# Optimization experiments

Hardware: AMD Instinct MI355X
Metric: run time of the kernel (lower is better)

The kernel has to match this reference:

```python
import jax, jax.numpy as jnp
import numpy as np

NV, NSEG, SEGSZ, GRID = 778, 16, 49, 32
SCALE_FACTOR = 0.1


def grid_sample_3d(vol, pts):
    """Trilinear grid_sample, align_corners=True, zeros padding.
    vol: [D,H,W]; pts: [N,3] with (x,y,z) in [-1,1] (x indexes W, z indexes D).
    """
    D, H, W = vol.shape
    fx = (pts[:, 0] + 1.0) * 0.5 * (W - 1)
    fy = (pts[:, 1] + 1.0) * 0.5 * (H - 1)
    fz = (pts[:, 2] + 1.0) * 0.5 * (D - 1)
    x0f, y0f, z0f = jnp.floor(fx), jnp.floor(fy), jnp.floor(fz)
    wx, wy, wz = fx - x0f, fy - y0f, fz - z0f
    x0 = x0f.astype(jnp.int32)
    y0 = y0f.astype(jnp.int32)
    z0 = z0f.astype(jnp.int32)
    out = jnp.zeros(pts.shape[0], vol.dtype)
    for dz in (0, 1):
        zz = z0 + dz
        ww_z = wz if dz else (1.0 - wz)
        for dy in (0, 1):
            yy = y0 + dy
            ww_zy = ww_z * (wy if dy else (1.0 - wy))
            for dx in (0, 1):
                xx = x0 + dx
                w = ww_zy * (wx if dx else (1.0 - wx))
                valid = (xx >= 0) & (xx < W) & (yy >= 0) & (yy < H) & (zz >= 0) & (zz < D)
                v = vol[jnp.clip(zz, 0, D - 1), jnp.clip(yy, 0, H - 1), jnp.clip(xx, 0, W - 1)]
                out = out + jnp.where(valid, v, 0.0) * w
    return out


def _boxes(segv):
    # segv: [B,16,S,3] -> center [B,16,3], scale [B,16]  (no_grad in original)
    mn = segv.min(axis=2)
    mx = segv.max(axis=2)
    center = 0.5 * (mn + mx)                       # mean of (min, max)
    scale = (1.0 + SCALE_FACTOR) * 0.5 * (mx - mn).max(axis=-1)
    return jax.lax.stop_gradient(center), jax.lax.stop_gradient(scale)


def _cross_sample(seg_src, center, scale, phi, seg):
    # seg_src [B,I,S,3]; center [B,J,3]; scale [B,J]; phi [J,B,G,G,G]
    B = seg_src.shape[0]
    coords = (seg_src[:, :, None, :, :] - center[:, None, :, None, :]) / scale[:, None, :, None, None]
    pts = coords.transpose(2, 0, 1, 3, 4).reshape(NSEG, B, NSEG * SEGSZ, 3)  # [J,B,M,3]
    vals = jax.vmap(jax.vmap(grid_sample_3d))(phi, pts)                      # [J,B,M]
    vals = vals.reshape(NSEG, B, NSEG, SEGSZ).transpose(1, 2, 0, 3)          # [B,I,J,S]
    phisum = vals.sum(axis=2)                                                # [B,I,S]
    orisum = (vals * scale[:, None, :, None]).sum(axis=2)                    # [B,I,S]
    flat = seg.reshape(-1)
    out = jnp.zeros((B, NV), jnp.float32).at[:, flat].add(phisum.reshape(B, -1))
    ori = jnp.zeros((B, NV), jnp.float32).at[:, flat].add(orisum.reshape(B, -1))
    return out, ori


def setup_inputs() -> dict:
    key = jax.random.key(0)
    k1, k2, k3, k4 = jax.random.split(key, 4)
    bs = 128
    vertices = jax.random.normal(k1, (bs, 2, NV, 3), dtype=jnp.float32)
    seg = jax.random.randint(k2, (NSEG, SEGSZ), 0, NV).astype(jnp.int32)
    phi_right = jax.random.uniform(k3, (NSEG, bs, GRID, GRID, GRID), dtype=jnp.float32)
    phi_left = jax.random.uniform(k4, (NSEG, bs, GRID, GRID, GRID), dtype=jnp.float32)
    return {"vertices": vertices, "phi_right": phi_right, "phi_left": phi_left, "seg": seg}


def reference(vertices, phi_right, phi_left, seg):
    left_vert = vertices[:, 1]   # [B,778,3]
    right_vert = vertices[:, 0]
    segL = left_vert[:, seg]     # [B,16,S,3]
    segR = right_vert[:, seg]
    cL, sL = _boxes(segL)
    cR, sR = _boxes(segR)
    out_left, _ = _cross_sample(segL, cR, sR, phi_right, seg)
    out_right, _ = _cross_sample(segR, cL, sL, phi_left, seg)
    num_hand = 2
    loss = (out_left / num_hand ** 2 + out_right / num_hand ** 2).sum(axis=1)  # [B]
    return loss
```

## Files before the change

kernel.cpp:

```cpp
#include <hip/hip_runtime.h>

#define NVV   778
#define NSEG  16
#define SEGSZ 49
#define GRIDN 32
#define BATCH 128
#define NPTS  (NSEG * SEGSZ)
#define VOLSZ (GRIDN * GRIDN * GRIDN)
#define NBLK  256
#define VPB   16

#define HF (16 * 1024)

typedef __attribute__((address_space(1))) const void* as1_t;
typedef __attribute__((address_space(3))) void* as3_t;

#define STREAM(DST, SRC) \
    { _Pragma("unroll") \
      for (int c_ = 0; c_ < 8; ++c_) { \
        int ch_ = c_ * 8 + wv; \
        __builtin_amdgcn_global_load_lds( \
            (as1_t)((SRC) + ch_ * 256 + lane * 4), \
            (as3_t)((DST) + ch_ * 256), 16, 0, 0); \
      } }

__device__ __forceinline__ float tapxy(const float* slab, int x0, int y0,
                                       float wx, float wy)
{
    float s = 0.f;
    #pragma unroll
    for (int dy = 0; dy < 2; ++dy) {
        int yy = y0 + dy;
        if (yy < 0 || yy >= GRIDN) continue;
        float wyv = dy ? wy : 1.f - wy;
        const float* row = slab + yy * GRIDN;
        #pragma unroll
        for (int dx = 0; dx < 2; ++dx) {
            int xx = x0 + dx;
            if (xx < 0 || xx >= GRIDN) continue;
            s += wyv * (dx ? wx : 1.f - wx) * row[xx];
        }
    }
    return s;
}

__global__ __launch_bounds__(1024, 4) void sample_kernel(
    const float* __restrict__ vertices, const int* __restrict__ seg,
    const float* __restrict__ phiR, const float* __restrict__ phiL,
    float* __restrict__ loss)
{
    __shared__ __align__(16) float B0[HF];
    __shared__ __align__(16) float B1[HF];
    __shared__ float4 sbox[VPB];
    __shared__ float wsum[8];

    const int tid  = threadIdx.x;
    const int bx   = blockIdx.x;
    const int k    = bx & (NSEG - 1);
    const int wv   = tid >> 6;
    const int lane = tid & 63;
    const bool producer = (wv < 8);
    const int ct   = tid - 512;

    auto phiPtr = [&](int it) {
        int vid  = bx + NBLK * it;
        int b    = (vid >> 4) & (BATCH - 1);
        int pass = vid >> 11;
        return (pass == 0 ? phiR : phiL) + ((size_t)k * BATCH + b) * VOLSZ;
    };
    auto vertBase = [&](int it) {
        int vid  = bx + NBLK * it;
        int b    = (vid >> 4) & (BATCH - 1);
        int srcS = (vid >> 11) == 0 ? 1 : 0;
        return vertices + ((size_t)b * 2 + srcS) * NVV * 3;
    };

    int pvi1 = 0, pvi2 = 0;
    bool has2 = false;
    if (!producer) {
        pvi1 = seg[ct];
        has2 = (ct + 512) < NPTS;
        pvi2 = has2 ? seg[ct + 512] : 0;
    }

    {
        int vidw    = bx + NBLK * wv;
        int bbw     = (vidw >> 4) & (BATCH - 1);
        int boxSide = ((vidw >> 11) == 0) ? 0 : 1;
        bool bact   = lane < SEGSZ;
        int bvi     = bact ? seg[k * SEGSZ + lane] : 0;
        const float* bvp = vertices + (((size_t)bbw * 2 + boxSide) * NVV + bvi) * 3;
        float x = bvp[0], y = bvp[1], z = bvp[2];
        float mnx = bact ? x : 1e30f, mxx = bact ? x : -1e30f;
        float mny = bact ? y : 1e30f, mxy = bact ? y : -1e30f;
        float mnz = bact ? z : 1e30f, mxz = bact ? z : -1e30f;
        #pragma unroll
        for (int m = 32; m; m >>= 1) {
            mnx = fminf(mnx, __shfl_xor(mnx, m));
            mxx = fmaxf(mxx, __shfl_xor(mxx, m));
            mny = fminf(mny, __shfl_xor(mny, m));
            mxy = fmaxf(mxy, __shfl_xor(mxy, m));
            mnz = fminf(mnz, __shfl_xor(mnz, m));
            mxz = fmaxf(mxz, __shfl_xor(mxz, m));
        }
        if (lane == 0) {
            float ext = fmaxf(fmaxf(mxx - mnx, mxy - mny), mxz - mnz);
            sbox[wv] = make_float4(0.5f * (mnx + mxx), 0.5f * (mny + mxy),
                                   0.5f * (mnz + mxz), 1.0f / (0.55f * ext));
        }
    }

    float p1x = 0.f, p1y = 0.f, p1z = 0.f;
    float p2x = 0.f, p2y = 0.f, p2z = 0.f;
    if (!producer) {
        const float* vb = vertBase(0);
        p1x = vb[pvi1 * 3 + 0]; p1y = vb[pvi1 * 3 + 1]; p1z = vb[pvi1 * 3 + 2];
        if (has2) {
            p2x = vb[pvi2 * 3 + 0]; p2y = vb[pvi2 * 3 + 1]; p2z = vb[pvi2 * 3 + 2];
        }
    }

    if (producer) { STREAM(B0, phiPtr(0)) }

    __syncthreads();

    float n1x = 0.f, n1y = 0.f, n1z = 0.f;
    float n2x = 0.f, n2y = 0.f, n2z = 0.f;

    for (int v = 0; v < VPB; ++v) {
        const bool more = (v + 1 < VPB);

        float f1x = 0.f, f1y = 0.f, f1z = -2.f;
        float f2x = 0.f, f2y = 0.f, f2z = -2.f;
        if (!producer) {
            float4 b4 = sbox[v];
            f1x = ((p1x - b4.x) * b4.w + 1.f) * 15.5f;
            f1y = ((p1y - b4.y) * b4.w + 1.f) * 15.5f;
            f1z = ((p1z - b4.z) * b4.w + 1.f) * 15.5f;
            if (has2) {
                f2x = ((p2x - b4.x) * b4.w + 1.f) * 15.5f;
                f2y = ((p2y - b4.y) * b4.w + 1.f) * 15.5f;
                f2z = ((p2z - b4.z) * b4.w + 1.f) * 15.5f;
            }
        }
        bool a1 = (f1x > -1.f && f1x < 32.f && f1y > -1.f && f1y < 32.f &&
                   f1z > -1.f && f1z < 32.f);
        bool a2 = (f2x > -1.f && f2x < 32.f && f2y > -1.f && f2y < 32.f &&
                   f2z > -1.f && f2z < 32.f);
        float x1f = floorf(f1x), y1f = floorf(f1y), z1f = floorf(f1z);
        float x2f = floorf(f2x), y2f = floorf(f2y), z2f = floorf(f2z);
        float w1x = f1x - x1f, w1y = f1y - y1f, w1z = f1z - z1f;
        float w2x = f2x - x2f, w2y = f2y - y2f, w2z = f2z - z2f;
        int x1 = (int)x1f, y1 = (int)y1f, z1 = (int)z1f;
        int x2 = (int)x2f, y2 = (int)y2f, z2 = (int)z2f;
        float acc1 = 0.f, acc2 = 0.f;

        if (producer) {
            STREAM(B1, phiPtr(v) + HF)
        } else {
            if (v > 0 && ct == 0) {
                float tot = 0.f;
                #pragma unroll
                for (int i = 0; i < 8; ++i) tot += wsum[i];
                int vidp = bx + NBLK * (v - 1);
                atomicAdd(loss + ((vidp >> 4) & (BATCH - 1)), tot * 0.25f);
            }
            if (a1 && z1 <= 15) {
                if (z1 >= 0)
                    acc1 += (1.f - w1z) * tapxy(B0 + z1 * 1024, x1, y1, w1x, w1y);
                if (z1 <= 14)
                    acc1 += w1z * tapxy(B0 + (z1 + 1) * 1024, x1, y1, w1x, w1y);
            }
            if (a2 && z2 <= 15) {
                if (z2 >= 0)
                    acc2 += (1.f - w2z) * tapxy(B0 + z2 * 1024, x2, y2, w2x, w2y);
                if (z2 <= 14)
                    acc2 += w2z * tapxy(B0 + (z2 + 1) * 1024, x2, y2, w2x, w2y);
            }
            if (more) {
                const float* vb = vertBase(v + 1);
                n1x = vb[pvi1 * 3 + 0]; n1y = vb[pvi1 * 3 + 1]; n1z = vb[pvi1 * 3 + 2];
                if (has2) {
                    n2x = vb[pvi2 * 3 + 0]; n2y = vb[pvi2 * 3 + 1]; n2z = vb[pvi2 * 3 + 2];
                }
            }
        }
        __syncthreads();

        if (producer) {
            if (more) { STREAM(B0, phiPtr(v + 1)) }
        } else {
            if (a1 && z1 >= 15) {
                if (z1 >= 16)
                    acc1 += (1.f - w1z) * tapxy(B1 + (z1 - 16) * 1024, x1, y1, w1x, w1y);
                if (z1 <= 30)
                    acc1 += w1z * tapxy(B1 + (z1 - 15) * 1024, x1, y1, w1x, w1y);
            }
            if (a2 && z2 >= 15) {
                if (z2 >= 16)
                    acc2 += (1.f - w2z) * tapxy(B1 + (z2 - 16) * 1024, x2, y2, w2x, w2y);
                if (z2 <= 30)
                    acc2 += w2z * tapxy(B1 + (z2 - 15) * 1024, x2, y2, w2x, w2y);
            }
            float acc = acc1 + acc2;
            #pragma unroll
            for (int off = 32; off; off >>= 1)
                acc += __shfl_down(acc, off);
            if (lane == 0) wsum[wv - 8] = acc;
        }
        __syncthreads();
        p1x = n1x; p1y = n1y; p1z = n1z;
        p2x = n2x; p2y = n2y; p2z = n2z;
    }

    if (!producer && ct == 0) {
        float tot = 0.f;
        #pragma unroll
        for (int i = 0; i < 8; ++i) tot += wsum[i];
        int vidp = bx + NBLK * (VPB - 1);
        atomicAdd(loss + ((vidp >> 4) & (BATCH - 1)), tot * 0.25f);
    }
}

extern "C" void kernel_launch(void* const* d_in, const int* in_sizes, int n_in,
                              void* d_out, int out_size, void* d_ws, size_t ws_size,
                              hipStream_t stream) {
    const float* vertices = (const float*)d_in[0];
    const float* phiR     = (const float*)d_in[1];
    const float* phiL     = (const float*)d_in[2];
    const int*   seg      = (const int*)d_in[3];
    float* loss = (float*)d_out;

    hipMemsetAsync(d_out, 0, (size_t)out_size * sizeof(float), stream);

    sample_kernel<<<NBLK, 1024, 0, stream>>>(vertices, seg, phiR, phiL, loss);
}
```

Before: 108.0 us.

## Split volume streaming into three LDS slabs with finer-grained async waits

The volume is now split into three z-slabs of 12, 12 and 8 planes held in three LDS buffers instead of two halves. Each slab is refilled as soon as consumers finish with it, and explicit vmcnt waits replace full __syncthreads. The aim is to overlap more of the global-to-LDS streaming with the sampling work and cut the stall at each barrier. The cost is an extra phase per volume and hand-managed waitcnt and barrier ordering, which risks races if the counts are wrong.

```diff
diff --git a/kernel.cpp b/kernel.cpp
--- a/kernel.cpp
+++ b/kernel.cpp
@@ -10,19 +10,25 @@
 #define NBLK  256
 #define VPB   16
 
-#define HF (16 * 1024)
+#define PF12 (12 * 1024)
 
 typedef __attribute__((address_space(1))) const void* as1_t;
 typedef __attribute__((address_space(3))) void* as3_t;
 
-#define STREAM(DST, SRC) \
+#define STREAM(DST, SRC, C) \
     { _Pragma("unroll") \
-      for (int c_ = 0; c_ < 8; ++c_) { \
+      for (int c_ = 0; c_ < (C); ++c_) { \
         int ch_ = c_ * 8 + wv; \
         __builtin_amdgcn_global_load_lds( \
             (as1_t)((SRC) + ch_ * 256 + lane * 4), \
             (as3_t)((DST) + ch_ * 256), 16, 0, 0); \
       } }
+
+#define WAITP(N) asm volatile("s_waitcnt vmcnt(" #N ")" ::: "memory");
+
+#define BAR { asm volatile("" ::: "memory"); \
+              __builtin_amdgcn_s_barrier(); \
+              asm volatile("" ::: "memory"); }
 
 __device__ __forceinline__ float tapxy(const float* slab, int x0, int y0,
                                        float wx, float wy)
@@ -44,13 +50,25 @@
     return s;
 }
 
+__device__ __forceinline__ void tap_pt(const float* bq, int q, bool act,
+    int z0, float wz, int x0, int y0, float wx, float wy, float& acc)
+{
+    if (!act) return;
+    if (z0 >= 0 && (z0 / 12) == q)
+        acc += (1.f - wz) * tapxy(bq + (z0 - 12 * q) * 1024, x0, y0, wx, wy);
+    int s = z0 + 1;
+    if (s <= 31 && (s / 12) == q)
+        acc += wz * tapxy(bq + (s - 12 * q) * 1024, x0, y0, wx, wy);
+}
+
 __global__ __launch_bounds__(1024, 4) void sample_kernel(
     const float* __restrict__ vertices, const int* __restrict__ seg,
     const float* __restrict__ phiR, const float* __restrict__ phiL,
     float* __restrict__ loss)
 {
-    __shared__ __align__(16) float B0[HF];
-    __shared__ __align__(16) float B1[HF];
+    __shared__ __align__(16) float B0[PF12];
+    __shared__ __align__(16) float B1[PF12];
+    __shared__ __align__(16) float B2[PF12];
     __shared__ float4 sbox[VPB];
     __shared__ float wsum[8];
 
@@ -120,7 +138,11 @@
         }
     }
 
-    if (producer) { STREAM(B0, phiPtr(0)) }
+    if (producer) {
+        const float* p0 = phiPtr(0);
+        STREAM(B0, p0, 6)
+        STREAM(B1, p0 + PF12, 6)
+    }
 
     __syncthreads();
 
@@ -156,7 +178,8 @@
         float acc1 = 0.f, acc2 = 0.f;
 
         if (producer) {
-            STREAM(B1, phiPtr(v) + HF)
+            STREAM(B2, phiPtr(v) + 2 * PF12, 4)
+            WAITP(4)
         } else {
             if (v > 0 && ct == 0) {
                 float tot = 0.f;
@@ -165,18 +188,21 @@
                 int vidp = bx + NBLK * (v - 1);
                 atomicAdd(loss + ((vidp >> 4) & (BATCH - 1)), tot * 0.25f);
             }
-            if (a1 && z1 <= 15) {
-                if (z1 >= 0)
-                    acc1 += (1.f - w1z) * tapxy(B0 + z1 * 1024, x1, y1, w1x, w1y);
-                if (z1 <= 14)
-                    acc1 += w1z * tapxy(B0 + (z1 + 1) * 1024, x1, y1, w1x, w1y);
-            }
-            if (a2 && z2 <= 15) {
-                if (z2 >= 0)
-                    acc2 += (1.f - w2z) * tapxy(B0 + z2 * 1024, x2, y2, w2x, w2y);
-                if (z2 <= 14)
-                    acc2 += w2z * tapxy(B0 + (z2 + 1) * 1024, x2, y2, w2x, w2y);
-            }
+            tap_pt(B0, 0, a1, z1, w1z, x1, y1, w1x, w1y, acc1);
+            tap_pt(B0, 0, a2, z2, w2z, x2, y2, w2x, w2y, acc2);
+        }
+        BAR
+
+        if (producer) {
+            if (more) {
+                STREAM(B0, phiPtr(v + 1), 6)
+                WAITP(6)
+            } else {
+                WAITP(0)
+            }
+        } else {
+            tap_pt(B1, 1, a1, z1, w1z, x1, y1, w1x, w1y, acc1);
+            tap_pt(B1, 1, a2, z2, w2z, x2, y2, w2x, w2y, acc2);
             if (more) {
                 const float* vb = vertBase(v + 1);
                 n1x = vb[pvi1 * 3 + 0]; n1y = vb[pvi1 * 3 + 1]; n1z = vb[pvi1 * 3 + 2];
@@ -185,30 +211,26 @@
                 }
             }
         }
-        __syncthreads();
+        BAR
 
         if (producer) {
-            if (more) { STREAM(B0, phiPtr(v + 1)) }
+            if (more) {
+                STREAM(B1, phiPtr(v + 1) + PF12, 6)
+                WAITP(6)
+            } else {
+                WAITP(0)
+            }
         } else {
-            if (a1 && z1 >= 15) {
-                if (z1 >= 16)
-                    acc1 += (1.f - w1z) * tapxy(B1 + (z1 - 16) * 1024, x1, y1, w1x, w1y);
-                if (z1 <= 30)
-                    acc1 += w1z * tapxy(B1 + (z1 - 15) * 1024, x1, y1, w1x, w1y);
-            }
-            if (a2 && z2 >= 15) {
-                if (z2 >= 16)
-                    acc2 += (1.f - w2z) * tapxy(B1 + (z2 - 16) * 1024, x2, y2, w2x, w2y);
-                if (z2 <= 30)
-                    acc2 += w2z * tapxy(B1 + (z2 - 15) * 1024, x2, y2, w2x, w2y);
-            }
+            tap_pt(B2, 2, a1, z1, w1z, x1, y1, w1x, w1y, acc1);
+            tap_pt(B2, 2, a2, z2, w2z, x2, y2, w2x, w2y, acc2);
             float acc = acc1 + acc2;
             #pragma unroll
             for (int off = 32; off; off >>= 1)
                 acc += __shfl_down(acc, off);
             if (lane == 0) wsum[wv - 8] = acc;
-        }
-        __syncthreads();
+            asm volatile("s_waitcnt lgkmcnt(0)" ::: "memory");
+        }
+        BAR
         p1x = n1x; p1y = n1y; p1z = n1z;
         p2x = n2x; p2y = n2y; p2z = n2z;
     }
```

New measurement: 107.9 us. Within noise of the previous version (-0.1%).

## Stage phi volumes through registers with nontemporal loads and deeper prefetch

Applied to the files above, without the earlier changes.

Replaces the direct global-to-LDS async loads with nontemporal dwordx4 loads into register staging buffers (two sets, X and Y). Producer waves write these to LDS after partial vmcnt waits, so the next half-volume can be in flight while the current one is written and consumed. The loop is restructured into a skewed half-step pipeline, with custom barriers that only wait on lgkmcnt. This adds register pressure on producers (64 extra VGPRs) and hand-written waitcnt sequencing, which risks ordering mistakes.

```diff
diff --git a/kernel.cpp b/kernel.cpp
--- a/kernel.cpp
+++ b/kernel.cpp
@@ -12,17 +12,40 @@
 
 #define HF (16 * 1024)
 
-typedef __attribute__((address_space(1))) const void* as1_t;
-typedef __attribute__((address_space(3))) void* as3_t;
-
-#define STREAM(DST, SRC) \
-    { _Pragma("unroll") \
-      for (int c_ = 0; c_ < 8; ++c_) { \
-        int ch_ = c_ * 8 + wv; \
-        __builtin_amdgcn_global_load_lds( \
-            (as1_t)((SRC) + ch_ * 256 + lane * 4), \
-            (as3_t)((DST) + ch_ * 256), 16, 0, 0); \
-      } }
+typedef float f4 __attribute__((ext_vector_type(4)));
+
+#define ISSUE(S, SRC) { \
+    const float* a_ = (SRC) + (wv << 11) + (lane << 2); \
+    const float* b_ = a_ + 1024; \
+    asm volatile("global_load_dwordx4 %0, %1, off nt"             : "=v"(S##0) : "v"(a_)); \
+    asm volatile("global_load_dwordx4 %0, %1, off offset:1024 nt" : "=v"(S##1) : "v"(a_)); \
+    asm volatile("global_load_dwordx4 %0, %1, off offset:2048 nt" : "=v"(S##2) : "v"(a_)); \
+    asm volatile("global_load_dwordx4 %0, %1, off offset:3072 nt" : "=v"(S##3) : "v"(a_)); \
+    asm volatile("global_load_dwordx4 %0, %1, off nt"             : "=v"(S##4) : "v"(b_)); \
+    asm volatile("global_load_dwordx4 %0, %1, off offset:1024 nt" : "=v"(S##5) : "v"(b_)); \
+    asm volatile("global_load_dwordx4 %0, %1, off offset:2048 nt" : "=v"(S##6) : "v"(b_)); \
+    asm volatile("global_load_dwordx4 %0, %1, off offset:3072 nt" : "=v"(S##7) : "v"(b_)); \
+}
+
+#define WAITV8 { asm volatile("s_waitcnt vmcnt(8)" ::: "memory"); \
+                 __builtin_amdgcn_sched_barrier(0); }
+#define WAITV0 { asm volatile("s_waitcnt vmcnt(0)" ::: "memory"); \
+                 __builtin_amdgcn_sched_barrier(0); }
+
+#define WRITE(DST, S) { \
+    float* d_ = (DST) + (wv << 11) + (lane << 2); \
+    *(f4*)(d_ +    0) = S##0; \
+    *(f4*)(d_ +  256) = S##1; \
+    *(f4*)(d_ +  512) = S##2; \
+    *(f4*)(d_ +  768) = S##3; \
+    *(f4*)(d_ + 1024) = S##4; \
+    *(f4*)(d_ + 1280) = S##5; \
+    *(f4*)(d_ + 1536) = S##6; \
+    *(f4*)(d_ + 1792) = S##7; }
+
+#define PBAR { asm volatile("s_waitcnt lgkmcnt(0)" ::: "memory"); \
+               __builtin_amdgcn_s_barrier(); \
+               asm volatile("" ::: "memory"); }
 
 __device__ __forceinline__ float tapxy(const float* slab, int x0, int y0,
                                        float wx, float wy)
@@ -74,6 +97,10 @@
         int srcS = (vid >> 11) == 0 ? 1 : 0;
         return vertices + ((size_t)b * 2 + srcS) * NVV * 3;
     };
+    auto bOf = [&](int it) { return (bx + NBLK * it) >> 4 & (BATCH - 1); };
+
+    f4 X0, X1, X2, X3, X4, X5, X6, X7;
+    f4 Y0, Y1, Y2, Y3, Y4, Y5, Y6, Y7;
 
     int pvi1 = 0, pvi2 = 0;
     bool has2 = false;
@@ -112,59 +139,86 @@
 
     float p1x = 0.f, p1y = 0.f, p1z = 0.f;
     float p2x = 0.f, p2y = 0.f, p2z = 0.f;
-    if (!producer) {
+    if (producer) {
+        ISSUE(X, phiPtr(0))
+    } else {
         const float* vb = vertBase(0);
         p1x = vb[pvi1 * 3 + 0]; p1y = vb[pvi1 * 3 + 1]; p1z = vb[pvi1 * 3 + 2];
         if (has2) {
             p2x = vb[pvi2 * 3 + 0]; p2y = vb[pvi2 * 3 + 1]; p2z = vb[pvi2 * 3 + 2];
         }
     }
-
-    if (producer) { STREAM(B0, phiPtr(0)) }
-
-    __syncthreads();
-
+    PBAR
+
+    bool a1 = false, a2 = false;
+    int x1 = 0, y1 = 0, z1 = 0, x2 = 0, y2 = 0, z2 = 0;
+    float w1x = 0.f, w1y = 0.f, w1z = 0.f, w2x = 0.f, w2y = 0.f, w2z = 0.f;
+    float acc1 = 0.f, acc2 = 0.f;
     float n1x = 0.f, n1y = 0.f, n1z = 0.f;
     float n2x = 0.f, n2y = 0.f, n2z = 0.f;
 
-    for (int v = 0; v < VPB; ++v) {
-        const bool more = (v + 1 < VPB);
-
-        float f1x = 0.f, f1y = 0.f, f1z = -2.f;
-        float f2x = 0.f, f2y = 0.f, f2z = -2.f;
-        if (!producer) {
-            float4 b4 = sbox[v];
-            f1x = ((p1x - b4.x) * b4.w + 1.f) * 15.5f;
-            f1y = ((p1y - b4.y) * b4.w + 1.f) * 15.5f;
-            f1z = ((p1z - b4.z) * b4.w + 1.f) * 15.5f;
-            if (has2) {
-                f2x = ((p2x - b4.x) * b4.w + 1.f) * 15.5f;
-                f2y = ((p2y - b4.y) * b4.w + 1.f) * 15.5f;
-                f2z = ((p2z - b4.z) * b4.w + 1.f) * 15.5f;
-            }
-        }
-        bool a1 = (f1x > -1.f && f1x < 32.f && f1y > -1.f && f1y < 32.f &&
-                   f1z > -1.f && f1z < 32.f);
-        bool a2 = (f2x > -1.f && f2x < 32.f && f2y > -1.f && f2y < 32.f &&
-                   f2z > -1.f && f2z < 32.f);
-        float x1f = floorf(f1x), y1f = floorf(f1y), z1f = floorf(f1z);
-        float x2f = floorf(f2x), y2f = floorf(f2y), z2f = floorf(f2z);
-        float w1x = f1x - x1f, w1y = f1y - y1f, w1z = f1z - z1f;
-        float w2x = f2x - x2f, w2y = f2y - y2f, w2z = f2z - z2f;
-        int x1 = (int)x1f, y1 = (int)y1f, z1 = (int)z1f;
-        int x2 = (int)x2f, y2 = (int)y2f, z2 = (int)z2f;
-        float acc1 = 0.f, acc2 = 0.f;
-
+    for (int h = 0; h <= 16; ++h) {
         if (producer) {
-            STREAM(B1, phiPtr(v) + HF)
+            if (h <= 15) {
+                ISSUE(Y, phiPtr(h) + HF)
+                WAITV8
+                WRITE(B0, X)
+            }
+        } else if (h >= 1) {
+            if (a1 && z1 >= 15) {
+                if (z1 >= 16)
+                    acc1 += (1.f - w1z) * tapxy(B1 + (z1 - 16) * 1024, x1, y1, w1x, w1y);
+                if (z1 <= 30)
+                    acc1 += w1z * tapxy(B1 + (z1 - 15) * 1024, x1, y1, w1x, w1y);
+            }
+            if (a2 && z2 >= 15) {
+                if (z2 >= 16)
+                    acc2 += (1.f - w2z) * tapxy(B1 + (z2 - 16) * 1024, x2, y2, w2x, w2y);
+                if (z2 <= 30)
+                    acc2 += w2z * tapxy(B1 + (z2 - 15) * 1024, x2, y2, w2x, w2y);
+            }
+            float acc = acc1 + acc2;
+            #pragma unroll
+            for (int off = 32; off; off >>= 1)
+                acc += __shfl_down(acc, off);
+            if (lane == 0) wsum[wv - 8] = acc;
+        }
+        PBAR
+        if (h == 16) break;
+
+        if (producer) {
+            if (h <= 14) {
+                ISSUE(X, phiPtr(h + 1))
+                WAITV8
+            } else {
+                WAITV0
+            }
+            WRITE(B1, Y)
         } else {
-            if (v > 0 && ct == 0) {
+            if (h >= 1 && ct == 0) {
                 float tot = 0.f;
                 #pragma unroll
                 for (int i = 0; i < 8; ++i) tot += wsum[i];
-                int vidp = bx + NBLK * (v - 1);
-                atomicAdd(loss + ((vidp >> 4) & (BATCH - 1)), tot * 0.25f);
-            }
+                atomicAdd(loss + bOf(h - 1), tot * 0.25f);
+            }
+            float4 b4 = sbox[h];
+            float f1x = ((p1x - b4.x) * b4.w + 1.f) * 15.5f;
+            float f1y = ((p1y - b4.y) * b4.w + 1.f) * 15.5f;
+            float f1z = ((p1z - b4.z) * b4.w + 1.f) * 15.5f;
+            float f2x = ((p2x - b4.x) * b4.w + 1.f) * 15.5f;
+            float f2y = ((p2y - b4.y) * b4.w + 1.f) * 15.5f;
+            float f2z = ((p2z - b4.z) * b4.w + 1.f) * 15.5f;
+            a1 = (f1x > -1.f && f1x < 32.f && f1y > -1.f && f1y < 32.f &&
+                  f1z > -1.f && f1z < 32.f);
+            a2 = has2 && (f2x > -1.f && f2x < 32.f && f2y > -1.f && f2y < 32.f &&
+                  f2z > -1.f && f2z < 32.f);
+            float x1f = floorf(f1x), y1f = floorf(f1y), z1f = floorf(f1z);
+            float x2f = floorf(f2x), y2f = floorf(f2y), z2f = floorf(f2z);
+            w1x = f1x - x1f; w1y = f1y - y1f; w1z = f1z - z1f;
+            w2x = f2x - x2f; w2y = f2y - y2f; w2z = f2z - z2f;
+            x1 = (int)x1f; y1 = (int)y1f; z1 = (int)z1f;
+            x2 = (int)x2f; y2 = (int)y2f; z2 = (int)z2f;
+            acc1 = 0.f; acc2 = 0.f;
             if (a1 && z1 <= 15) {
                 if (z1 >= 0)
                     acc1 += (1.f - w1z) * tapxy(B0 + z1 * 1024, x1, y1, w1x, w1y);
@@ -177,48 +231,24 @@
                 if (z2 <= 14)
                     acc2 += w2z * tapxy(B0 + (z2 + 1) * 1024, x2, y2, w2x, w2y);
             }
-            if (more) {
-                const float* vb = vertBase(v + 1);
+            if (h <= 14) {
+                const float* vb = vertBase(h + 1);
                 n1x = vb[pvi1 * 3 + 0]; n1y = vb[pvi1 * 3 + 1]; n1z = vb[pvi1 * 3 + 2];
                 if (has2) {
                     n2x = vb[pvi2 * 3 + 0]; n2y = vb[pvi2 * 3 + 1]; n2z = vb[pvi2 * 3 + 2];
                 }
             }
-        }
-        __syncthreads();
-
-        if (producer) {
-            if (more) { STREAM(B0, phiPtr(v + 1)) }
-        } else {
-            if (a1 && z1 >= 15) {
-                if (z1 >= 16)
-                    acc1 += (1.f - w1z) * tapxy(B1 + (z1 - 16) * 1024, x1, y1, w1x, w1y);
-                if (z1 <= 30)
-                    acc1 += w1z * tapxy(B1 + (z1 - 15) * 1024, x1, y1, w1x, w1y);
-            }
-            if (a2 && z2 >= 15) {
-                if (z2 >= 16)
-                    acc2 += (1.f - w2z) * tapxy(B1 + (z2 - 16) * 1024, x2, y2, w2x, w2y);
-                if (z2 <= 30)
-                    acc2 += w2z * tapxy(B1 + (z2 - 15) * 1024, x2, y2, w2x, w2y);
-            }
-            float acc = acc1 + acc2;
-            #pragma unroll
-            for (int off = 32; off; off >>= 1)
-                acc += __shfl_down(acc, off);
-            if (lane == 0) wsum[wv - 8] = acc;
-        }
-        __syncthreads();
-        p1x = n1x; p1y = n1y; p1z = n1z;
-        p2x = n2x; p2y = n2y; p2z = n2z;
+            p1x = n1x; p1y = n1y; p1z = n1z;
+            p2x = n2x; p2y = n2y; p2z = n2z;
+        }
+        PBAR
     }
 
     if (!producer && ct == 0) {
         float tot = 0.f;
         #pragma unroll
         for (int i = 0; i < 8; ++i) tot += wsum[i];
-        int vidp = bx + NBLK * (VPB - 1);
-        atomicAdd(loss + ((vidp >> 4) & (BATCH - 1)), tot * 0.25f);
+        atomicAdd(loss + bOf(VPB - 1), tot * 0.25f);
     }
 }
 
```

Result: no change. 108.0 us (+0.0%).
